# Kernel tuning notes

Measured on AMD Instinct MI355X. Metric: run time of the kernel, lower is better.

The kernel has to match this reference:

```python
import jax, jax.numpy as jnp
import numpy as np

EPS = 1e-5

def group_norm(x, gamma, beta, groups):
    # x: (B, C, D, H, W)
    B, C = x.shape[0], x.shape[1]
    xr = x.reshape(B, groups, C // groups, -1)
    mean = xr.mean(axis=(2, 3), keepdims=True)
    var = xr.var(axis=(2, 3), keepdims=True)
    xn = ((xr - mean) * jax.lax.rsqrt(var + EPS)).reshape(x.shape)
    return xn * gamma[None, :, None, None, None] + beta[None, :, None, None, None]

def setup_inputs() -> dict:
    key = jax.random.key(0)
    ks = jax.random.split(key, 8)
    B, Ccls = 2, 32
    D = H = W = 64
    s = 0.05
    return {
        "x": jax.random.normal(ks[0], (B, 768, 8, 8, 8), jnp.float32),
        "out": jax.random.normal(ks[1], (B, 48, D, H, W), jnp.float32),
        "task_encoding": jax.random.normal(ks[2], (Ccls, 256, 1, 1, 1), jnp.float32),
        "gn1_g": jnp.ones((768,), jnp.float32),
        "gn1_b": jnp.zeros((768,), jnp.float32),
        "gap_w": jax.random.normal(ks[3], (256, 768), jnp.float32) * s,
        "gap_b": jnp.zeros((256,), jnp.float32),
        "ctrl_w": jax.random.normal(ks[4], (153, 512), jnp.float32) * s,
        "ctrl_b": jnp.zeros((153,), jnp.float32),
        "gn2_g": jnp.ones((48,), jnp.float32),
        "gn2_b": jnp.zeros((48,), jnp.float32),
        "pre_w": jax.random.normal(ks[5], (8, 48), jnp.float32) * s,
        "pre_b": jnp.zeros((8,), jnp.float32),
    }

def reference(x, out, task_encoding, gn1_g, gn1_b, gap_w, gap_b, ctrl_w, ctrl_b,
              gn2_g, gn2_b, pre_w, pre_b):
    B = x.shape[0]
    Ccls = task_encoding.shape[0]
    # GAP branch: GroupNorm(16,768) -> ReLU -> global avg pool -> 1x1x1 conv 768->256
    h = jax.nn.relu(group_norm(x, gn1_g, gn1_b, 16))
    pooled = h.mean(axis=(2, 3, 4))                       # (B, 768)
    x_feat = pooled @ gap_w.T + gap_b                     # (B, 256)
    # Controller: per (batch, class) params from concat(x_feat, task_encoding)
    te = task_encoding.reshape(Ccls, -1)                  # (Ccls, 256)
    params = (jnp.einsum('pf,bf->bp', ctrl_w[:, :256], x_feat)[:, None, :]
              + jnp.einsum('pf,cf->cp', ctrl_w[:, 256:], te)[None, :, :]
              + ctrl_b)                                   # (B, Ccls, 153)
    w1 = params[..., 0:64].reshape(B, Ccls, 8, 8)
    w2 = params[..., 64:128].reshape(B, Ccls, 8, 8)
    w3 = params[..., 128:136].reshape(B, Ccls, 1, 8)
    b1 = params[..., 136:144]
    b2 = params[..., 144:152]
    b3 = params[..., 152:153]
    # precls branch: GroupNorm(16,48) -> ReLU -> 1x1x1 conv 48->8
    g = jax.nn.relu(group_norm(out, gn2_g, gn2_b, 16))
    h0 = jnp.einsum('oc,bcdhw->bodhw', pre_w, g) + pre_b[None, :, None, None, None]
    # Dynamic per-class head: 8->8->8->1 pointwise MLP with ReLU between layers
    t = jax.nn.relu(jnp.einsum('bcij,bjdhw->bcidhw', w1, h0) + b1[..., None, None, None])
    t = jax.nn.relu(jnp.einsum('bcij,bcjdhw->bcidhw', w2, t) + b2[..., None, None, None])
    logits = jnp.einsum('bcij,bcjdhw->bcidhw', w3, t) + b3[..., None, None, None]
    # (B, Ccls, 1, D, H, W) -> (B, Ccls, D, H, W)
    return logits[:, :, 0]
```

## Files before the change

### kernel.cpp

```cpp
#include <hip/hip_runtime.h>

constexpr int NCLS = 32;

constexpr int WS_POOL = 64;
constexpr int WS_PAR = 2112;
constexpr int WS_P2  = 11904;

__device__ __forceinline__ float wred(float v) {
#pragma unroll
  for (int off = 32; off > 0; off >>= 1) v += __shfl_down(v, off, 64);
  return v;
}

__global__ void k_gn2_part(const float* __restrict__ o, float* __restrict__ ws) {
  int blk = blockIdx.x;
  const float4* p = reinterpret_cast<const float4*>(o + (size_t)blk * 32768);
  float s = 0.f, s2 = 0.f;
#pragma unroll
  for (int k = 0; k < 32; ++k) {
    float4 v = p[k * 256 + threadIdx.x];
    s  += v.x + v.y + v.z + v.w;
    s2 += v.x*v.x + v.y*v.y + v.z*v.z + v.w*v.w;
  }
  s = wred(s); s2 = wred(s2);
  __shared__ float red[8];
  int wid = threadIdx.x >> 6, lane = threadIdx.x & 63;
  if (lane == 0) { red[wid*2] = s; red[wid*2+1] = s2; }
  __syncthreads();
  if (threadIdx.x == 0) {
    ws[WS_P2 + blk*2]   = red[0]+red[2]+red[4]+red[6];
    ws[WS_P2 + blk*2+1] = red[1]+red[3]+red[5]+red[7];
  }
}

__global__ void k1_gn1_pool(const float* __restrict__ x, const float* __restrict__ g1,
                            const float* __restrict__ b1, float* __restrict__ ws) {
  int g = blockIdx.x;
  int t = threadIdx.x;
  const float4* p = reinterpret_cast<const float4*>(x + g * 24576);
  float s = 0.f, s2 = 0.f;
#pragma unroll
  for (int k = 0; k < 24; ++k) {
    float4 v = p[k * 256 + t];
    s  += v.x + v.y + v.z + v.w;
    s2 += v.x*v.x + v.y*v.y + v.z*v.z + v.w*v.w;
  }
  s = wred(s); s2 = wred(s2);
  __shared__ float red[8];
  __shared__ float mstat[2];
  int wid = t >> 6, lane = t & 63;
  if (lane == 0) { red[wid*2] = s; red[wid*2+1] = s2; }
  __syncthreads();
  if (t == 0) {
    float S  = red[0]+red[2]+red[4]+red[6];
    float S2 = red[1]+red[3]+red[5]+red[7];
    float mean = S * (1.f/24576.f);
    float var  = S2 * (1.f/24576.f) - mean*mean;
    mstat[0] = mean; mstat[1] = rsqrtf(var + 1e-5f);
  }
  __syncthreads();
  float mean = mstat[0], rstd = mstat[1];
#pragma unroll
  for (int k = 0; k < 12; ++k) {
    int i = k*4 + wid;
    int c = (g & 15) * 48 + i;
    float sc = rstd * g1[c];
    float sh = b1[c] - mean * sc;
    const float* q = x + g * 24576 + i * 512;
    float acc = 0.f;
#pragma unroll
    for (int j = 0; j < 8; ++j)
      acc += fmaxf(fmaf(q[lane + j*64], sc, sh), 0.f);
    acc = wred(acc);
    if (lane == 0) ws[WS_POOL + (g >> 4) * 768 + c] = acc * (1.f/512.f);
  }
}

__global__ void k2_params(const float* __restrict__ gapw, const float* __restrict__ gapb,
                          const float* __restrict__ cw, const float* __restrict__ cb,
                          const float* __restrict__ te, float* __restrict__ ws) {
  int b = blockIdx.x >> 5, cls = blockIdx.x & 31;
  int t = threadIdx.x;
  __shared__ __align__(16) float pl[768];
  __shared__ __align__(16) float tl[256];
  __shared__ __align__(16) float xl[256];
  pl[t] = ws[WS_POOL + b*768 + t];
  pl[t+256] = ws[WS_POOL + b*768 + t + 256];
  pl[t+512] = ws[WS_POOL + b*768 + t + 512];
  tl[t] = te[cls*256 + t];
  __syncthreads();
  {
    float acc = gapb[t];
    const float4* w4 = reinterpret_cast<const float4*>(gapw) + t * 192;
    const float4* p4 = reinterpret_cast<const float4*>(pl);
#pragma unroll 4
    for (int jj = 0; jj < 192; ++jj) {
      float4 w = w4[jj], p = p4[jj];
      acc = fmaf(w.x, p.x, acc); acc = fmaf(w.y, p.y, acc);
      acc = fmaf(w.z, p.z, acc); acc = fmaf(w.w, p.w, acc);
    }
    xl[t] = acc;
  }
  __syncthreads();
  if (t < 153) {
    float a = cb[t];
    const float4* c4 = reinterpret_cast<const float4*>(cw) + t * 128;
    const float4* x4 = reinterpret_cast<const float4*>(xl);
    const float4* t4 = reinterpret_cast<const float4*>(tl);
#pragma unroll 4
    for (int jj = 0; jj < 64; ++jj) {
      float4 w = c4[jj], v = x4[jj];
      a = fmaf(w.x, v.x, a); a = fmaf(w.y, v.y, a);
      a = fmaf(w.z, v.z, a); a = fmaf(w.w, v.w, a);
    }
#pragma unroll 4
    for (int jj = 0; jj < 64; ++jj) {
      float4 w = c4[64 + jj], v = t4[jj];
      a = fmaf(w.x, v.x, a); a = fmaf(w.y, v.y, a);
      a = fmaf(w.z, v.z, a); a = fmaf(w.w, v.w, a);
    }
    ws[WS_PAR + (b*NCLS + cls)*153 + t] = a;
  }
}

__global__ __launch_bounds__(256) void k4_main(const float* __restrict__ oin,
                                               const float* __restrict__ prew,
                                               const float* __restrict__ preb,
                                               const float* __restrict__ g2,
                                               const float* __restrict__ b2,
                                               const float* __restrict__ ws,
                                               float* __restrict__ out) {
  __shared__ __align__(16) float Wl[NCLS * 160];
  __shared__ float prewT[384];
  __shared__ float2 ssl[48];
  __shared__ float ms[64];
  int t = threadIdx.x;
  int b = blockIdx.x >> 8, tile = blockIdx.x & 255;

  if (t < 32) {
    float S = 0.f, S2 = 0.f;
#pragma unroll
    for (int k = 0; k < 24; ++k) {
      S  += ws[WS_P2 + (t*24 + k)*2];
      S2 += ws[WS_P2 + (t*24 + k)*2 + 1];
    }
    float mean = S * (1.f/786432.f);
    float var  = S2 * (1.f/786432.f) - mean*mean;
    ms[t*2] = mean; ms[t*2+1] = rsqrtf(var + 1e-5f);
  }
  if (t < 128) {
#pragma unroll
    for (int k = 0; k < 3; ++k) {
      int i = t + k*128;
      prewT[(i % 48) * 8 + (i / 48)] = prew[i];
    }
  }
  {
    const float* wsrc = ws + WS_PAR + b * (NCLS*153);
#pragma unroll 4
    for (int cc = 0; cc < NCLS; ++cc)
      if (t < 153) Wl[cc*160 + t] = wsrc[cc*153 + t];
  }
  __syncthreads();
  if (t < 48) {
    int grp = (b << 4) + t / 3;
    float mean = ms[grp*2], rstd = ms[grp*2+1];
    float sc = rstd * g2[t];
    ssl[t] = make_float2(sc, b2[t] - mean * sc);
  }
  __syncthreads();

  const float4* ip4 = reinterpret_cast<const float4*>(oin) + (size_t)b * 48 * 65536 + tile*256 + t;
  float4 h0[8];
#pragma unroll
  for (int o = 0; o < 8; ++o) { float pb = preb[o]; h0[o] = make_float4(pb, pb, pb, pb); }
#pragma unroll
  for (int c = 0; c < 48; ++c) {
    float4 v = ip4[(size_t)c * 65536];
    float2 ss = ssl[c];
    float4 g;
    g.x = fmaxf(fmaf(v.x, ss.x, ss.y), 0.f);
    g.y = fmaxf(fmaf(v.y, ss.x, ss.y), 0.f);
    g.z = fmaxf(fmaf(v.z, ss.x, ss.y), 0.f);
    g.w = fmaxf(fmaf(v.w, ss.x, ss.y), 0.f);
#pragma unroll
    for (int o = 0; o < 8; ++o) {
      float w = prewT[c*8 + o];
      h0[o].x = fmaf(w, g.x, h0[o].x);
      h0[o].y = fmaf(w, g.y, h0[o].y);
      h0[o].z = fmaf(w, g.z, h0[o].z);
      h0[o].w = fmaf(w, g.w, h0[o].w);
    }
  }

  float4* op4 = reinterpret_cast<float4*>(out) + (size_t)b * NCLS * 65536 + tile*256 + t;
#pragma unroll 1
  for (int cls = 0; cls < NCLS; ++cls) {
    const float* W = Wl + cls * 160;
    float4 t1[8], t2[8];
#pragma unroll
    for (int i = 0; i < 8; ++i) {
      float bias = W[136 + i];
      float4 a = make_float4(bias, bias, bias, bias);
#pragma unroll
      for (int j = 0; j < 8; ++j) {
        float w = W[i*8 + j];
        a.x = fmaf(w, h0[j].x, a.x); a.y = fmaf(w, h0[j].y, a.y);
        a.z = fmaf(w, h0[j].z, a.z); a.w = fmaf(w, h0[j].w, a.w);
      }
      t1[i].x = fmaxf(a.x, 0.f); t1[i].y = fmaxf(a.y, 0.f);
      t1[i].z = fmaxf(a.z, 0.f); t1[i].w = fmaxf(a.w, 0.f);
    }
#pragma unroll
    for (int i = 0; i < 8; ++i) {
      float bias = W[144 + i];
      float4 a = make_float4(bias, bias, bias, bias);
#pragma unroll
      for (int j = 0; j < 8; ++j) {
        float w = W[64 + i*8 + j];
        a.x = fmaf(w, t1[j].x, a.x); a.y = fmaf(w, t1[j].y, a.y);
        a.z = fmaf(w, t1[j].z, a.z); a.w = fmaf(w, t1[j].w, a.w);
      }
      t2[i].x = fmaxf(a.x, 0.f); t2[i].y = fmaxf(a.y, 0.f);
      t2[i].z = fmaxf(a.z, 0.f); t2[i].w = fmaxf(a.w, 0.f);
    }
    float b3v = W[152];
    float4 lg = make_float4(b3v, b3v, b3v, b3v);
#pragma unroll
    for (int j = 0; j < 8; ++j) {
      float w = W[128 + j];
      lg.x = fmaf(w, t2[j].x, lg.x); lg.y = fmaf(w, t2[j].y, lg.y);
      lg.z = fmaf(w, t2[j].z, lg.z); lg.w = fmaf(w, t2[j].w, lg.w);
    }
    op4[(size_t)cls * 65536] = lg;
  }
}

extern "C" void kernel_launch(void* const* d_in, const int* in_sizes, int n_in,
                              void* d_out, int out_size, void* d_ws, size_t ws_size,
                              hipStream_t stream) {
  const float* x    = (const float*)d_in[0];
  const float* oin  = (const float*)d_in[1];
  const float* te   = (const float*)d_in[2];
  const float* g1   = (const float*)d_in[3];
  const float* b1   = (const float*)d_in[4];
  const float* gapw = (const float*)d_in[5];
  const float* gapb = (const float*)d_in[6];
  const float* cw   = (const float*)d_in[7];
  const float* cb   = (const float*)d_in[8];
  const float* g2   = (const float*)d_in[9];
  const float* b2   = (const float*)d_in[10];
  const float* prew = (const float*)d_in[11];
  const float* preb = (const float*)d_in[12];
  float* ws  = (float*)d_ws;
  float* out = (float*)d_out;

  hipLaunchKernelGGL(k_gn2_part,  dim3(768), dim3(256), 0, stream, oin, ws);
  hipLaunchKernelGGL(k1_gn1_pool, dim3(32),  dim3(256), 0, stream, x, g1, b1, ws);
  hipLaunchKernelGGL(k2_params,   dim3(64),  dim3(256), 0, stream, gapw, gapb, cw, cb, te, ws);
  hipLaunchKernelGGL(k4_main,     dim3(512), dim3(256), 0, stream, oin, prew, preb, g2, b2, ws, out);
}
```

Before: 314.8 us.

## Merge stats kernels, split param GEMV into wave-per-output kernels, double voxels per thread

```diff
diff --git a/kernel.cpp b/kernel.cpp
--- a/kernel.cpp
+++ b/kernel.cpp
@@ -3,6 +3,7 @@
 constexpr int NCLS = 32;
 
 constexpr int WS_POOL = 64;
+constexpr int WS_XF  = 1600;
 constexpr int WS_PAR = 2112;
 constexpr int WS_P2  = 11904;
 
@@ -12,115 +13,116 @@
   return v;
 }
 
-__global__ void k_gn2_part(const float* __restrict__ o, float* __restrict__ ws) {
-  int blk = blockIdx.x;
-  const float4* p = reinterpret_cast<const float4*>(o + (size_t)blk * 32768);
-  float s = 0.f, s2 = 0.f;
-#pragma unroll
-  for (int k = 0; k < 32; ++k) {
-    float4 v = p[k * 256 + threadIdx.x];
-    s  += v.x + v.y + v.z + v.w;
-    s2 += v.x*v.x + v.y*v.y + v.z*v.z + v.w*v.w;
-  }
-  s = wred(s); s2 = wred(s2);
+__device__ __forceinline__ float4 fma4(float w, float4 v, float4 a) {
+  a.x = fmaf(w, v.x, a.x); a.y = fmaf(w, v.y, a.y);
+  a.z = fmaf(w, v.z, a.z); a.w = fmaf(w, v.w, a.w);
+  return a;
+}
+__device__ __forceinline__ float4 relu4(float4 a) {
+  a.x = fmaxf(a.x, 0.f); a.y = fmaxf(a.y, 0.f);
+  a.z = fmaxf(a.z, 0.f); a.w = fmaxf(a.w, 0.f);
+  return a;
+}
+__device__ __forceinline__ float4 bcast4(float v) { return make_float4(v, v, v, v); }
+
+__global__ void k1_stats(const float* __restrict__ x, const float* __restrict__ oin,
+                         const float* __restrict__ g1, const float* __restrict__ b1,
+                         float* __restrict__ ws) {
+  int t = threadIdx.x;
+  int wid = t >> 6, lane = t & 63;
   __shared__ float red[8];
+  if (blockIdx.x < 768) {
+    int blk = blockIdx.x;
+    const float4* p = reinterpret_cast<const float4*>(oin + (size_t)blk * 32768);
+    float s = 0.f, s2 = 0.f;
+#pragma unroll
+    for (int k = 0; k < 32; ++k) {
+      float4 v = p[k * 256 + t];
+      s  += v.x + v.y + v.z + v.w;
+      s2 += v.x*v.x + v.y*v.y + v.z*v.z + v.w*v.w;
+    }
+    s = wred(s); s2 = wred(s2);
+    if (lane == 0) { red[wid*2] = s; red[wid*2+1] = s2; }
+    __syncthreads();
+    if (t == 0) {
+      ws[WS_P2 + blk*2]   = red[0]+red[2]+red[4]+red[6];
+      ws[WS_P2 + blk*2+1] = red[1]+red[3]+red[5]+red[7];
+    }
+  } else {
+    int g = blockIdx.x - 768;
+    __shared__ float mstat[2];
+    const float4* p = reinterpret_cast<const float4*>(x + g * 24576);
+    float s = 0.f, s2 = 0.f;
+#pragma unroll
+    for (int k = 0; k < 24; ++k) {
+      float4 v = p[k * 256 + t];
+      s  += v.x + v.y + v.z + v.w;
+      s2 += v.x*v.x + v.y*v.y + v.z*v.z + v.w*v.w;
+    }
+    s = wred(s); s2 = wred(s2);
+    if (lane == 0) { red[wid*2] = s; red[wid*2+1] = s2; }
+    __syncthreads();
+    if (t == 0) {
+      float S  = red[0]+red[2]+red[4]+red[6];
+      float S2 = red[1]+red[3]+red[5]+red[7];
+      float mean = S * (1.f/24576.f);
+      float var  = S2 * (1.f/24576.f) - mean*mean;
+      mstat[0] = mean; mstat[1] = rsqrtf(var + 1e-5f);
+    }
+    __syncthreads();
+    float mean = mstat[0], rstd = mstat[1];
+#pragma unroll
+    for (int k = 0; k < 12; ++k) {
+      int i = k*4 + wid;
+      int c = (g & 15) * 48 + i;
+      float sc = rstd * g1[c];
+      float sh = b1[c] - mean * sc;
+      const float* q = x + g * 24576 + i * 512;
+      float acc = 0.f;
+#pragma unroll
+      for (int j = 0; j < 8; ++j)
+        acc += fmaxf(fmaf(q[lane + j*64], sc, sh), 0.f);
+      acc = wred(acc);
+      if (lane == 0) ws[WS_POOL + (g >> 4) * 768 + c] = acc * (1.f/512.f);
+    }
+  }
+}
+
+__global__ void k2_xfeat(const float* __restrict__ gapw, const float* __restrict__ gapb,
+                         float* __restrict__ ws) {
   int wid = threadIdx.x >> 6, lane = threadIdx.x & 63;
-  if (lane == 0) { red[wid*2] = s; red[wid*2+1] = s2; }
-  __syncthreads();
-  if (threadIdx.x == 0) {
-    ws[WS_P2 + blk*2]   = red[0]+red[2]+red[4]+red[6];
-    ws[WS_P2 + blk*2+1] = red[1]+red[3]+red[5]+red[7];
-  }
-}
-
-__global__ void k1_gn1_pool(const float* __restrict__ x, const float* __restrict__ g1,
-                            const float* __restrict__ b1, float* __restrict__ ws) {
-  int g = blockIdx.x;
-  int t = threadIdx.x;
-  const float4* p = reinterpret_cast<const float4*>(x + g * 24576);
-  float s = 0.f, s2 = 0.f;
-#pragma unroll
-  for (int k = 0; k < 24; ++k) {
-    float4 v = p[k * 256 + t];
-    s  += v.x + v.y + v.z + v.w;
-    s2 += v.x*v.x + v.y*v.y + v.z*v.z + v.w*v.w;
-  }
-  s = wred(s); s2 = wred(s2);
-  __shared__ float red[8];
-  __shared__ float mstat[2];
-  int wid = t >> 6, lane = t & 63;
-  if (lane == 0) { red[wid*2] = s; red[wid*2+1] = s2; }
-  __syncthreads();
-  if (t == 0) {
-    float S  = red[0]+red[2]+red[4]+red[6];
-    float S2 = red[1]+red[3]+red[5]+red[7];
-    float mean = S * (1.f/24576.f);
-    float var  = S2 * (1.f/24576.f) - mean*mean;
-    mstat[0] = mean; mstat[1] = rsqrtf(var + 1e-5f);
-  }
-  __syncthreads();
-  float mean = mstat[0], rstd = mstat[1];
-#pragma unroll
-  for (int k = 0; k < 12; ++k) {
-    int i = k*4 + wid;
-    int c = (g & 15) * 48 + i;
-    float sc = rstd * g1[c];
-    float sh = b1[c] - mean * sc;
-    const float* q = x + g * 24576 + i * 512;
-    float acc = 0.f;
-#pragma unroll
-    for (int j = 0; j < 8; ++j)
-      acc += fmaxf(fmaf(q[lane + j*64], sc, sh), 0.f);
-    acc = wred(acc);
-    if (lane == 0) ws[WS_POOL + (g >> 4) * 768 + c] = acc * (1.f/512.f);
-  }
-}
-
-__global__ void k2_params(const float* __restrict__ gapw, const float* __restrict__ gapb,
-                          const float* __restrict__ cw, const float* __restrict__ cb,
+  int idx = blockIdx.x * 4 + wid;
+  int b = idx >> 8, o = idx & 255;
+  const float* pw = gapw + o * 768;
+  const float* pp = ws + WS_POOL + b * 768;
+  float s = 0.f;
+#pragma unroll
+  for (int i = 0; i < 12; ++i) {
+    int cc = lane + i*64;
+    s += pw[cc] * pp[cc];
+  }
+  s = wred(s);
+  if (lane == 0) ws[WS_XF + idx] = s + gapb[o];
+}
+
+__global__ void k3_params(const float* __restrict__ cw, const float* __restrict__ cb,
                           const float* __restrict__ te, float* __restrict__ ws) {
-  int b = blockIdx.x >> 5, cls = blockIdx.x & 31;
-  int t = threadIdx.x;
-  __shared__ __align__(16) float pl[768];
-  __shared__ __align__(16) float tl[256];
-  __shared__ __align__(16) float xl[256];
-  pl[t] = ws[WS_POOL + b*768 + t];
-  pl[t+256] = ws[WS_POOL + b*768 + t + 256];
-  pl[t+512] = ws[WS_POOL + b*768 + t + 512];
-  tl[t] = te[cls*256 + t];
-  __syncthreads();
-  {
-    float acc = gapb[t];
-    const float4* w4 = reinterpret_cast<const float4*>(gapw) + t * 192;
-    const float4* p4 = reinterpret_cast<const float4*>(pl);
-#pragma unroll 4
-    for (int jj = 0; jj < 192; ++jj) {
-      float4 w = w4[jj], p = p4[jj];
-      acc = fmaf(w.x, p.x, acc); acc = fmaf(w.y, p.y, acc);
-      acc = fmaf(w.z, p.z, acc); acc = fmaf(w.w, p.w, acc);
-    }
-    xl[t] = acc;
-  }
-  __syncthreads();
-  if (t < 153) {
-    float a = cb[t];
-    const float4* c4 = reinterpret_cast<const float4*>(cw) + t * 128;
-    const float4* x4 = reinterpret_cast<const float4*>(xl);
-    const float4* t4 = reinterpret_cast<const float4*>(tl);
-#pragma unroll 4
-    for (int jj = 0; jj < 64; ++jj) {
-      float4 w = c4[jj], v = x4[jj];
-      a = fmaf(w.x, v.x, a); a = fmaf(w.y, v.y, a);
-      a = fmaf(w.z, v.z, a); a = fmaf(w.w, v.w, a);
-    }
-#pragma unroll 4
-    for (int jj = 0; jj < 64; ++jj) {
-      float4 w = c4[64 + jj], v = t4[jj];
-      a = fmaf(w.x, v.x, a); a = fmaf(w.y, v.y, a);
-      a = fmaf(w.z, v.z, a); a = fmaf(w.w, v.w, a);
-    }
-    ws[WS_PAR + (b*NCLS + cls)*153 + t] = a;
-  }
+  int wid = threadIdx.x >> 6, lane = threadIdx.x & 63;
+  int e = blockIdx.x * 4 + wid;
+  int b = e / (NCLS * 153);
+  int r = e % (NCLS * 153);
+  int c = r / 153, p = r % 153;
+  const float* w  = cw + p * 512;
+  const float* xf = ws + WS_XF + b * 256;
+  const float* tv = te + c * 256;
+  float s = 0.f;
+#pragma unroll
+  for (int i = 0; i < 4; ++i) {
+    int f = lane + i*64;
+    s += w[f] * xf[f] + w[256 + f] * tv[f];
+  }
+  s = wred(s);
+  if (lane == 0) ws[WS_PAR + e] = s + cb[p];
 }
 
 __global__ __launch_bounds__(256) void k4_main(const float* __restrict__ oin,
@@ -131,11 +133,11 @@
                                                const float* __restrict__ ws,
                                                float* __restrict__ out) {
   __shared__ __align__(16) float Wl[NCLS * 160];
-  __shared__ float prewT[384];
+  __shared__ __align__(16) float prewT[384];
   __shared__ float2 ssl[48];
   __shared__ float ms[64];
   int t = threadIdx.x;
-  int b = blockIdx.x >> 8, tile = blockIdx.x & 255;
+  int b = blockIdx.x >> 7, tile = blockIdx.x & 127;
 
   if (t < 32) {
     float S = 0.f, S2 = 0.f;
@@ -170,69 +172,78 @@
   }
   __syncthreads();
 
-  const float4* ip4 = reinterpret_cast<const float4*>(oin) + (size_t)b * 48 * 65536 + tile*256 + t;
-  float4 h0[8];
-#pragma unroll
-  for (int o = 0; o < 8; ++o) { float pb = preb[o]; h0[o] = make_float4(pb, pb, pb, pb); }
+  const float4* ip4 = reinterpret_cast<const float4*>(oin)
+                      + (size_t)b * 48 * 65536 + tile*512 + t;
+  const float4* pT4 = reinterpret_cast<const float4*>(prewT);
+  float4 h0a[8], h0b[8];
+#pragma unroll
+  for (int o = 0; o < 8; ++o) { float pb = preb[o]; h0a[o] = bcast4(pb); h0b[o] = bcast4(pb); }
 #pragma unroll
   for (int c = 0; c < 48; ++c) {
-    float4 v = ip4[(size_t)c * 65536];
+    float4 va = ip4[(size_t)c * 65536];
+    float4 vb = ip4[(size_t)c * 65536 + 256];
     float2 ss = ssl[c];
-    float4 g;
-    g.x = fmaxf(fmaf(v.x, ss.x, ss.y), 0.f);
-    g.y = fmaxf(fmaf(v.y, ss.x, ss.y), 0.f);
-    g.z = fmaxf(fmaf(v.z, ss.x, ss.y), 0.f);
-    g.w = fmaxf(fmaf(v.w, ss.x, ss.y), 0.f);
-#pragma unroll
-    for (int o = 0; o < 8; ++o) {
-      float w = prewT[c*8 + o];
-      h0[o].x = fmaf(w, g.x, h0[o].x);
-      h0[o].y = fmaf(w, g.y, h0[o].y);
-      h0[o].z = fmaf(w, g.z, h0[o].z);
-      h0[o].w = fmaf(w, g.w, h0[o].w);
-    }
-  }
-
-  float4* op4 = reinterpret_cast<float4*>(out) + (size_t)b * NCLS * 65536 + tile*256 + t;
+    float4 ga = relu4(make_float4(fmaf(va.x, ss.x, ss.y), fmaf(va.y, ss.x, ss.y),
+                                  fmaf(va.z, ss.x, ss.y), fmaf(va.w, ss.x, ss.y)));
+    float4 gb = relu4(make_float4(fmaf(vb.x, ss.x, ss.y), fmaf(vb.y, ss.x, ss.y),
+                                  fmaf(vb.z, ss.x, ss.y), fmaf(vb.w, ss.x, ss.y)));
+    float4 w0 = pT4[c*2], w1 = pT4[c*2+1];
+    h0a[0] = fma4(w0.x, ga, h0a[0]); h0b[0] = fma4(w0.x, gb, h0b[0]);
+    h0a[1] = fma4(w0.y, ga, h0a[1]); h0b[1] = fma4(w0.y, gb, h0b[1]);
+    h0a[2] = fma4(w0.z, ga, h0a[2]); h0b[2] = fma4(w0.z, gb, h0b[2]);
+    h0a[3] = fma4(w0.w, ga, h0a[3]); h0b[3] = fma4(w0.w, gb, h0b[3]);
+    h0a[4] = fma4(w1.x, ga, h0a[4]); h0b[4] = fma4(w1.x, gb, h0b[4]);
+    h0a[5] = fma4(w1.y, ga, h0a[5]); h0b[5] = fma4(w1.y, gb, h0b[5]);
+    h0a[6] = fma4(w1.z, ga, h0a[6]); h0b[6] = fma4(w1.z, gb, h0b[6]);
+    h0a[7] = fma4(w1.w, ga, h0a[7]); h0b[7] = fma4(w1.w, gb, h0b[7]);
+  }
+
+  float4* op4 = reinterpret_cast<float4*>(out)
+                + (size_t)b * NCLS * 65536 + tile*512 + t;
 #pragma unroll 1
   for (int cls = 0; cls < NCLS; ++cls) {
-    const float* W = Wl + cls * 160;
-    float4 t1[8], t2[8];
+    const float4* W4 = reinterpret_cast<const float4*>(Wl + cls * 160);
+    float4 b1q0 = W4[34], b1q1 = W4[35];
+    float4 b2q0 = W4[36], b2q1 = W4[37];
+    float4 w3q0 = W4[32], w3q1 = W4[33];
+    float b3v = W4[38].x;
+    float b1arr[8] = {b1q0.x,b1q0.y,b1q0.z,b1q0.w,b1q1.x,b1q1.y,b1q1.z,b1q1.w};
+    float b2arr[8] = {b2q0.x,b2q0.y,b2q0.z,b2q0.w,b2q1.x,b2q1.y,b2q1.z,b2q1.w};
+    float w3arr[8] = {w3q0.x,w3q0.y,w3q0.z,w3q0.w,w3q1.x,w3q1.y,w3q1.z,w3q1.w};
+
+    float4 t1a[8], t1b[8];
 #pragma unroll
     for (int i = 0; i < 8; ++i) {
-      float bias = W[136 + i];
-      float4 a = make_float4(bias, bias, bias, bias);
-#pragma unroll
-      for (int j = 0; j < 8; ++j) {
-        float w = W[i*8 + j];
-        a.x = fmaf(w, h0[j].x, a.x); a.y = fmaf(w, h0[j].y, a.y);
-        a.z = fmaf(w, h0[j].z, a.z); a.w = fmaf(w, h0[j].w, a.w);
-      }
-      t1[i].x = fmaxf(a.x, 0.f); t1[i].y = fmaxf(a.y, 0.f);
-      t1[i].z = fmaxf(a.z, 0.f); t1[i].w = fmaxf(a.w, 0.f);
-    }
+      float4 w0 = W4[i*2], w1 = W4[i*2+1];
+      float4 aA = bcast4(b1arr[i]), aB = bcast4(b1arr[i]);
+      aA = fma4(w0.x, h0a[0], aA); aB = fma4(w0.x, h0b[0], aB);
+      aA = fma4(w0.y, h0a[1], aA); aB = fma4(w0.y, h0b[1], aB);
+      aA = fma4(w0.z, h0a[2], aA); aB = fma4(w0.z, h0b[2], aB);
+      aA = fma4(w0.w, h0a[3], aA); aB = fma4(w0.w, h0b[3], aB);
+      aA = fma4(w1.x, h0a[4], aA); aB = fma4(w1.x, h0b[4], aB);
+      aA = fma4(w1.y, h0a[5], aA); aB = fma4(w1.y, h0b[5], aB);
+      aA = fma4(w1.z, h0a[6], aA); aB = fma4(w1.z, h0b[6], aB);
+      aA = fma4(w1.w, h0a[7], aA); aB = fma4(w1.w, h0b[7], aB);
+      t1a[i] = relu4(aA); t1b[i] = relu4(aB);
+    }
+    float4 lgA = bcast4(b3v), lgB = bcast4(b3v);
 #pragma unroll
     for (int i = 0; i < 8; ++i) {
-      float bias = W[144 + i];
-      float4 a = make_float4(bias, bias, bias, bias);
-#pragma unroll
-      for (int j = 0; j < 8; ++j) {
-        float w = W[64 + i*8 + j];
-        a.x = fmaf(w, t1[j].x, a.x); a.y = fmaf(w, t1[j].y, a.y);
-        a.z = fmaf(w, t1[j].z, a.z); a.w = fmaf(w, t1[j].w, a.w);
-      }
-      t2[i].x = fmaxf(a.x, 0.f); t2[i].y = fmaxf(a.y, 0.f);
-      t2[i].z = fmaxf(a.z, 0.f); t2[i].w = fmaxf(a.w, 0.f);
-    }
-    float b3v = W[152];
-    float4 lg = make_float4(b3v, b3v, b3v, b3v);
-#pragma unroll
-    for (int j = 0; j < 8; ++j) {
-      float w = W[128 + j];
-      lg.x = fmaf(w, t2[j].x, lg.x); lg.y = fmaf(w, t2[j].y, lg.y);
-      lg.z = fmaf(w, t2[j].z, lg.z); lg.w = fmaf(w, t2[j].w, lg.w);
-    }
-    op4[(size_t)cls * 65536] = lg;
+      float4 w0 = W4[16 + i*2], w1 = W4[17 + i*2];
+      float4 aA = bcast4(b2arr[i]), aB = bcast4(b2arr[i]);
+      aA = fma4(w0.x, t1a[0], aA); aB = fma4(w0.x, t1b[0], aB);
+      aA = fma4(w0.y, t1a[1], aA); aB = fma4(w0.y, t1b[1], aB);
+      aA = fma4(w0.z, t1a[2], aA); aB = fma4(w0.z, t1b[2], aB);
+      aA = fma4(w0.w, t1a[3], aA); aB = fma4(w0.w, t1b[3], aB);
+      aA = fma4(w1.x, t1a[4], aA); aB = fma4(w1.x, t1b[4], aB);
+      aA = fma4(w1.y, t1a[5], aA); aB = fma4(w1.y, t1b[5], aB);
+      aA = fma4(w1.z, t1a[6], aA); aB = fma4(w1.z, t1b[6], aB);
+      aA = fma4(w1.w, t1a[7], aA); aB = fma4(w1.w, t1b[7], aB);
+      aA = relu4(aA); aB = relu4(aB);
+      lgA = fma4(w3arr[i], aA, lgA); lgB = fma4(w3arr[i], aB, lgB);
+    }
+    op4[(size_t)cls * 65536]       = lgA;
+    op4[(size_t)cls * 65536 + 256] = lgB;
   }
 }
 
@@ -255,8 +266,8 @@
   float* ws  = (float*)d_ws;
   float* out = (float*)d_out;
 
-  hipLaunchKernelGGL(k_gn2_part,  dim3(768), dim3(256), 0, stream, oin, ws);
-  hipLaunchKernelGGL(k1_gn1_pool, dim3(32),  dim3(256), 0, stream, x, g1, b1, ws);
-  hipLaunchKernelGGL(k2_params,   dim3(64),  dim3(256), 0, stream, gapw, gapb, cw, cb, te, ws);
-  hipLaunchKernelGGL(k4_main,     dim3(512), dim3(256), 0, stream, oin, prew, preb, g2, b2, ws, out);
-}
+  hipLaunchKernelGGL(k1_stats,  dim3(800),  dim3(256), 0, stream, x, oin, g1, b1, ws);
+  hipLaunchKernelGGL(k2_xfeat,  dim3(128),  dim3(256), 0, stream, gapw, gapb, ws);
+  hipLaunchKernelGGL(k3_params, dim3(2448), dim3(256), 0, stream, cw, cb, te, ws);
+  hipLaunchKernelGGL(k4_main,   dim3(256),  dim3(256), 0, stream, oin, prew, preb, g2, b2, ws, out);
+}
```

After: 284.1 us. 9.8% less time.
